# Kernel optimization log

Measured on AMD Instinct MI355X. Metric: run time of the kernel, lower is better.

The kernel has to match this reference:

```python
import jax, jax.numpy as jnp
import numpy as np
import math

B, S, D, H = 2, 2048, 2048, 16
HD = D // H  # 128


def _rope(x, cos, sin):
    # x: [b, s, h, hd]; cos/sin: [s, hd//2]
    # torch view_as_complex pairs adjacent elements: (even=real, odd=imag)
    xr = x[..., 0::2]
    xi = x[..., 1::2]
    c = cos[None, :, None, :]
    s = sin[None, :, None, :]
    out_r = xr * c - xi * s
    out_i = xr * s + xi * c
    # interleave back: [..., hd//2, 2] -> [..., hd]
    return jnp.stack([out_r, out_i], axis=-1).reshape(x.shape)


def setup_inputs() -> dict:
    key = jax.random.key(0)
    ks = jax.random.split(key, 5)
    x = jax.random.normal(ks[0], (B, S, D), dtype=jnp.float32)
    std = 1.0 / math.sqrt(D)
    wq = jax.random.normal(ks[1], (D, D), dtype=jnp.float32) * std
    wk = jax.random.normal(ks[2], (D, D), dtype=jnp.float32) * std
    wv = jax.random.normal(ks[3], (D, D), dtype=jnp.float32) * std
    wo = jax.random.normal(ks[4], (D, D), dtype=jnp.float32) * std
    # RoPE frequencies, theta = 10000
    freqs = 1.0 / (10000.0 ** (jnp.arange(0, HD, 2, dtype=jnp.float32) / HD))  # [hd//2]
    t = jnp.arange(S, dtype=jnp.float32)
    angles = jnp.outer(t, freqs)  # [s, hd//2]
    freqs_cos = jnp.cos(angles)
    freqs_sin = jnp.sin(angles)
    # causal additive mask [s, s]
    mask = jnp.triu(jnp.full((S, S), -jnp.inf, dtype=jnp.float32), k=1)
    return {"x": x, "start_pos": 0, "freqs_cos": freqs_cos, "freqs_sin": freqs_sin,
            "mask": mask, "wq": wq, "wk": wk, "wv": wv, "wo": wo}


def reference(x, start_pos, freqs_cos, freqs_sin, mask, wq, wk, wv, wo):
    b, s, d = x.shape
    # projections (torch Linear: y = x @ W.T)
    xq = (x @ wq.T).reshape(b, s, H, HD)
    xk = (x @ wk.T).reshape(b, s, H, HD)
    xv = (x @ wv.T).reshape(b, s, H, HD)
    xq = _rope(xq, freqs_cos, freqs_sin)
    xk = _rope(xk, freqs_cos, freqs_sin)
    # start_pos = 0 prefill: cache[:b, :s] == freshly computed xk/xv
    # scores: [b, h, s_q, s_k]
    scores = jnp.einsum("bqhd,bkhd->bhqk", xq, xk) / math.sqrt(HD)
    scores = scores + mask[None, None, :, :]
    probs = jax.nn.softmax(scores, axis=-1)
    out = jnp.einsum("bhqk,bkhd->bqhd", probs, xv).reshape(b, s, d)
    return out @ wo.T
```

## Files before the change

kernel.cpp:

```cpp
#include <hip/hip_runtime.h>

typedef __attribute__((ext_vector_type(8))) short short8;
typedef __attribute__((ext_vector_type(4))) float f32x4;
typedef __attribute__((ext_vector_type(16))) float f32x16;
typedef unsigned int u32;
typedef __attribute__((ext_vector_type(4))) u32 u32x4;
typedef unsigned short u16;

#define DEV __device__ __forceinline__

DEV void async16(const void* g, void* l) {
  __builtin_amdgcn_global_load_lds((const __attribute__((address_space(1))) u32*)g,
                                   (__attribute__((address_space(3))) u32*)l, 16, 0, 0);
}

DEV u16 f2bf(float f) {
  u32 u = __builtin_bit_cast(u32, f);
  u32 r = (u + 0x7FFFu + ((u >> 16) & 1u)) >> 16;
  return (u16)r;
}
DEV float bf2f(u16 h) { return __builtin_bit_cast(float, (u32)h << 16); }

DEV u32 cvtpk(float lo, float hi) {
  u32 r;
  asm("v_cvt_pk_bf16_f32 %0, %1, %2" : "=v"(r) : "v"(lo), "v"(hi));
  return r;
}

#define RAW_BARRIER() asm volatile("s_barrier" ::: "memory")
#define VMWAIT(N) asm volatile("s_waitcnt vmcnt(" #N ")" ::: "memory")

__global__ void cast_all_kernel(const float* __restrict__ x, const float* __restrict__ wq,
                                const float* __restrict__ wk, const float* __restrict__ wv,
                                const float* __restrict__ wo, u16* __restrict__ out) {
  constexpr int XN = 2097152;
  constexpr int WN = 1048576;
  constexpr int TOT = XN + 4 * WN;
  int stride = gridDim.x * blockDim.x;
  for (int i = blockIdx.x * blockDim.x + threadIdx.x; i < TOT; i += stride) {
    const float* src;
    int off;
    if (i < XN) {
      src = x; off = i;
    } else {
      int j = i - XN, wsel = j >> 20;
      const float* ws4[4] = {wq, wk, wv, wo};
      src = ws4[wsel]; off = j & (WN - 1);
    }
    float4 v = reinterpret_cast<const float4*>(src)[off];
    ushort4 o = make_ushort4(f2bf(v.x), f2bf(v.y), f2bf(v.z), f2bf(v.w));
    reinterpret_cast<ushort4*>(out)[i] = o;
  }
}

__global__ __launch_bounds__(512, 2) void gemm_qkv8(const u16* __restrict__ A,
                                                    const u16* __restrict__ Bw,
                                                    u16* __restrict__ q_ws,
                                                    u16* __restrict__ k_ws,
                                                    u16* __restrict__ vt_ws,
                                                    const float* __restrict__ cbp,
                                                    const float* __restrict__ sbp) {
  constexpr int K = 2048, NITER = 16;
  __shared__ char sm[131072];
  const int tid = threadIdx.x, lane = tid & 63, w = tid >> 6;
  const int wm = w >> 2, wn = w & 3;
  const int bid = blockIdx.x;
  const int xcd = bid & 7, jj = bid >> 3;
  const int mt = (xcd & 1) * 8 + (jj & 7);
  const int ntc = (xcd >> 1) * 6 + (jj >> 3);
  const int row0 = mt * 256, col0 = ntc * 256;

  f32x4 acc[2][2][4][2] = {};

  auto stage = [&](int slotbase, const u16* src, int rbase, int k0) {
#pragma unroll
    for (int i = 0; i < 2; ++i) {
      int slot = tid + i * 512;
      int r = slot >> 3, cs = slot & 7;
      async16(src + (size_t)(rbase + r) * K + k0 + ((cs ^ (r & 7)) << 3),
              sm + slotbase + slot * 16);
    }
  };

  short8 af[4][2], bf0[2][2], bf1[2][2];
  auto ldA = [&](int slotbase) {
#pragma unroll
    for (int mi = 0; mi < 4; ++mi) {
      int row = wm * 64 + mi * 16 + (lane & 15);
#pragma unroll
      for (int kk = 0; kk < 2; ++kk)
        af[mi][kk] = *reinterpret_cast<const short8*>(
            sm + slotbase + row * 128 + ((((kk << 2) + (lane >> 4)) ^ (row & 7)) << 4));
    }
  };
  auto ldB = [&](short8 (&bf)[2][2], int slotbase) {
#pragma unroll
    for (int ni = 0; ni < 2; ++ni) {
      int row = wn * 32 + ni * 16 + (lane & 15);
#pragma unroll
      for (int kk = 0; kk < 2; ++kk)
        bf[ni][kk] = *reinterpret_cast<const short8*>(
            sm + slotbase + row * 128 + ((((kk << 2) + (lane >> 4)) ^ (row & 7)) << 4));
    }
  };

#define MFMA16(HA, HB, BF)                                                              \
  __builtin_amdgcn_s_setprio(1);                                                        \
  _Pragma("unroll") for (int mi = 0; mi < 4; ++mi)                                      \
      _Pragma("unroll") for (int ni = 0; ni < 2; ++ni)                                  \
          _Pragma("unroll") for (int kk = 0; kk < 2; ++kk)                              \
              acc[HA][HB][mi][ni] = __builtin_amdgcn_mfma_f32_16x16x32_bf16(            \
                  af[mi][kk], BF[ni][kk], acc[HA][HB][mi][ni], 0, 0, 0);                \
  __builtin_amdgcn_s_setprio(0);

  stage(0, A, row0, 0);
  stage(32768, Bw, col0, 0);
  stage(49152, Bw, col0 + 128, 0);
  stage(16384, A, row0 + 128, 0);
  stage(65536, A, row0, 64);
  stage(65536 + 32768, Bw, col0, 64);

  for (int i = 0; i < NITER - 1; ++i) {
    const int kT1 = i * 128 + 64, kN = (i + 1) * 128;
    VMWAIT(8); RAW_BARRIER();
    ldA(0); ldB(bf0, 32768);
    stage(65536 + 49152, Bw, col0 + 128, kT1);
    MFMA16(0, 0, bf0);
    VMWAIT(8); RAW_BARRIER();
    ldB(bf1, 49152);
    stage(65536 + 16384, A, row0 + 128, kT1);
    MFMA16(0, 1, bf1);
    VMWAIT(8); RAW_BARRIER();
    ldA(16384);
    stage(0, A, row0, kN);
    stage(32768, Bw, col0, kN);
    MFMA16(1, 0, bf0);
    MFMA16(1, 1, bf1);
    VMWAIT(8); RAW_BARRIER();
    ldA(65536); ldB(bf0, 65536 + 32768);
    stage(49152, Bw, col0 + 128, kN);
    MFMA16(0, 0, bf0);
    VMWAIT(8); RAW_BARRIER();
    ldB(bf1, 65536 + 49152);
    stage(16384, A, row0 + 128, kN);
    MFMA16(0, 1, bf1);
    VMWAIT(8); RAW_BARRIER();
    ldA(65536 + 16384);
    stage(65536, A, row0, kN + 64);
    stage(65536 + 32768, Bw, col0, kN + 64);
    MFMA16(1, 0, bf0);
    MFMA16(1, 1, bf1);
  }
  {
    const int kT1 = (NITER - 1) * 128 + 64;
    VMWAIT(8); RAW_BARRIER();
    ldA(0); ldB(bf0, 32768);
    stage(65536 + 49152, Bw, col0 + 128, kT1);
    MFMA16(0, 0, bf0);
    VMWAIT(8); RAW_BARRIER();
    ldB(bf1, 49152);
    stage(65536 + 16384, A, row0 + 128, kT1);
    MFMA16(0, 1, bf1);
    VMWAIT(8); RAW_BARRIER();
    ldA(16384);
    MFMA16(1, 0, bf0);
    MFMA16(1, 1, bf1);
    VMWAIT(4); RAW_BARRIER();
    ldA(65536); ldB(bf0, 65536 + 32768);
    MFMA16(0, 0, bf0);
    VMWAIT(2); RAW_BARRIER();
    ldB(bf1, 65536 + 49152);
    MFMA16(0, 1, bf1);
    VMWAIT(0); RAW_BARRIER();
    ldA(65536 + 16384);
    MFMA16(1, 0, bf0);
    MFMA16(1, 1, bf1);
  }

  const float rs = 0.127517436f;
#pragma unroll
  for (int ha = 0; ha < 2; ++ha)
#pragma unroll
    for (int hb = 0; hb < 2; ++hb)
#pragma unroll
      for (int mi = 0; mi < 4; ++mi)
#pragma unroll
        for (int ni = 0; ni < 2; ++ni)
#pragma unroll
          for (int rr = 0; rr < 4; ++rr) {
            int gm = row0 + ha * 128 + wm * 64 + mi * 16 + ((lane >> 4) << 2) + rr;
            int gn = col0 + hb * 128 + wn * 32 + ni * 16 + (lane & 15);
            float v = acc[ha][hb][mi][ni][rr];
            int tsel = gn >> 11, nn = gn & 2047;
            int b = gm >> 11, s = gm & 2047, h = nn >> 7, hd = nn & 127;
            if (tsel < 2) {
              float pv = __shfl_xor(v, 1, 64);
              float c = cbp[(s << 6) + (hd >> 1)];
              float sn = sbp[(s << 6) + (hd >> 1)];
              float o = (hd & 1) ? (pv * sn + v * c) : (v * c - pv * sn);
              if (tsel == 0) o *= rs;
              u16* dst = tsel ? k_ws : q_ws;
              dst[(size_t)((b << 4) | h) * 262144 + (s << 7) + hd] = f2bf(o);
            } else {
              vt_ws[(size_t)((b << 4) | h) * 262144 + (hd << 11) + s] = f2bf(v);
            }
          }
#undef MFMA16
}

__global__ __launch_bounds__(256) void gemm_bt(const u16* __restrict__ A,
                                               const u16* __restrict__ Bw,
                                               float* __restrict__ C) {
  constexpr int K = 2048;
  __shared__ char sm[32768];
  const int tid = threadIdx.x;
  const int lane = tid & 63;
  const int w = tid >> 6;
  const int by = blockIdx.x & 31;
  const int bx = blockIdx.x >> 5;
  const int row0 = by * 128, col0 = bx * 128;
  const int wr = (w >> 1) * 64, wc = (w & 1) * 64;
  f32x4 acc[4][4] = {};

  for (int k0 = 0; k0 < K; k0 += 64) {
    __syncthreads();
#pragma unroll
    for (int i = 0; i < 4; ++i) {
      int slot = tid + i * 256;
      int r = slot >> 3, s = slot & 7;
      int sl = s ^ (r & 7);
      async16(A + (size_t)(row0 + r) * K + (k0 + sl * 8), sm + slot * 16);
    }
#pragma unroll
    for (int i = 0; i < 4; ++i) {
      int slot = tid + i * 256;
      int r = slot >> 3, s = slot & 7;
      int sl = s ^ (r & 7);
      async16(Bw + (size_t)(col0 + r) * K + (k0 + sl * 8), sm + 16384 + slot * 16);
    }
    __syncthreads();
#pragma unroll
    for (int kk = 0; kk < 2; ++kk) {
      short8 af[4], bfr[4];
#pragma unroll
      for (int mi = 0; mi < 4; ++mi) {
        int r = wr + mi * 16 + (lane & 15);
        int ps = (kk * 4 + (lane >> 4)) ^ (r & 7);
        af[mi] = *reinterpret_cast<const short8*>(sm + r * 128 + ps * 16);
      }
#pragma unroll
      for (int ni = 0; ni < 4; ++ni) {
        int r = wc + ni * 16 + (lane & 15);
        int ps = (kk * 4 + (lane >> 4)) ^ (r & 7);
        bfr[ni] = *reinterpret_cast<const short8*>(sm + 16384 + r * 128 + ps * 16);
      }
#pragma unroll
      for (int mi = 0; mi < 4; ++mi)
#pragma unroll
        for (int ni = 0; ni < 4; ++ni)
          acc[mi][ni] = __builtin_amdgcn_mfma_f32_16x16x32_bf16(af[mi], bfr[ni], acc[mi][ni], 0, 0, 0);
    }
  }
#pragma unroll
  for (int mi = 0; mi < 4; ++mi)
#pragma unroll
    for (int ni = 0; ni < 4; ++ni)
#pragma unroll
      for (int r = 0; r < 4; ++r) {
        int gm = row0 + wr + mi * 16 + ((lane >> 4) << 2) + r;
        int gn = col0 + wc + ni * 16 + (lane & 15);
        C[((size_t)gm << 11) + gn] = acc[mi][ni][r];
      }
}

__global__ __launch_bounds__(256, 2) void attn_kernel(const u16* __restrict__ q_ws,
                                                      const u16* __restrict__ k_ws,
                                                      const u16* __restrict__ vt_ws,
                                                      u16* __restrict__ attn_ws) {
  constexpr int S = 2048;
  constexpr float NEGBIG = -3.0e38f;
  __shared__ char sm[65536];
  const int tid = threadIdx.x, lane = tid & 63, w = tid >> 6;
  const int hi = lane >> 5, l31 = lane & 31;
  const int bid = blockIdx.x;
  const int qtr = bid >> 5;
  const int qt = (qtr < 8) ? qtr : 23 - qtr;
  const int bh = ((bid & 7) << 2) | ((bid >> 3) & 3);
  const int qr0 = qt * 128 + w * 32;
  const int ntile = 2 * qt + 2;
  const int my_nt = (qr0 >> 6) + 1;

  const u16* qp = q_ws + (size_t)bh * S * 128;
  const u16* kp = k_ws + (size_t)bh * S * 128;
  const u16* vp = vt_ws + (size_t)bh * 128 * S;

  short8 qf[8];
  {
    const u16* qr = qp + (size_t)(qr0 + l31) * 128 + hi * 8;
#pragma unroll
    for (int ks = 0; ks < 8; ++ks) qf[ks] = *reinterpret_cast<const short8*>(qr + ks * 16);
  }
  f32x16 accO[4];
#pragma unroll
  for (int dc = 0; dc < 4; ++dc)
#pragma unroll
    for (int r = 0; r < 16; ++r) accO[dc][r] = 0.f;
  float m = -1e30f, l = 0.f;

  auto stage = [&](int bufoff, int kv0) {
#pragma unroll
    for (int i = 0; i < 4; ++i) {
      int slot = tid + i * 256;
      int r = slot >> 4, s = slot & 15;
      async16(kp + (size_t)(kv0 + r) * 128 + ((s ^ (r & 15)) * 8), sm + bufoff + slot * 16);
    }
#pragma unroll
    for (int i = 0; i < 4; ++i) {
      int slot = tid + i * 256;
      int r = slot >> 3, s = slot & 7;
      async16(vp + (size_t)r * S + kv0 + ((s ^ (r & 7)) * 8), sm + bufoff + 16384 + slot * 16);
    }
  };

  stage(0, 0);
  __syncthreads();

  for (int t = 0; t < ntile; ++t) {
    const char* kb = sm + (t & 1) * 32768;
    const char* vb = kb + 16384;
    if (t + 1 < ntile) stage(((t + 1) & 1) * 32768, (t + 1) * 64);

    if (t < my_nt) {
      f32x16 sacc[2];
#pragma unroll
      for (int jc = 0; jc < 2; ++jc)
#pragma unroll
        for (int r = 0; r < 16; ++r) sacc[jc][r] = 0.f;
      __builtin_amdgcn_s_setprio(1);
#pragma unroll
      for (int jc = 0; jc < 2; ++jc) {
        const char* krp = kb + (jc * 32 + l31) * 256;
        const int sw = l31 & 15;
#pragma unroll
        for (int ks = 0; ks < 8; ++ks) {
          short8 kf = *reinterpret_cast<const short8*>(krp + (((2 * ks + hi) ^ sw) << 4));
          sacc[jc] = __builtin_amdgcn_mfma_f32_32x32x16_bf16(kf, qf[ks], sacc[jc], 0, 0, 0);
        }
      }
      __builtin_amdgcn_s_setprio(0);
      if (t == my_nt - 1) {
#pragma unroll
        for (int jc = 0; jc < 2; ++jc) {
          int thr = qr0 + l31 - t * 64 - 32 * jc - 4 * hi;
#pragma unroll
          for (int r = 0; r < 16; ++r) {
            int c0 = (r & 3) + 8 * (r >> 2);
            if (c0 > thr) sacc[jc][r] = NEGBIG;
          }
        }
      }
      float pmA = NEGBIG, pmB = NEGBIG, pmC = NEGBIG, pmD = NEGBIG;
#pragma unroll
      for (int jc = 0; jc < 2; ++jc)
#pragma unroll
        for (int r = 0; r < 16; r += 4) {
          pmA = fmaxf(pmA, sacc[jc][r]);
          pmB = fmaxf(pmB, sacc[jc][r + 1]);
          pmC = fmaxf(pmC, sacc[jc][r + 2]);
          pmD = fmaxf(pmD, sacc[jc][r + 3]);
        }
      float pmax = fmaxf(fmaxf(pmA, pmB), fmaxf(pmC, pmD));
      pmax = fmaxf(pmax, __shfl_xor(pmax, 32, 64));
      if (!__all(pmax - m <= 8.0f)) {
        float mnew = fmaxf(m, pmax);
        float scl = exp2f(m - mnew);
        m = mnew;
        l *= scl;
#pragma unroll
        for (int dc = 0; dc < 4; ++dc)
#pragma unroll
          for (int r = 0; r < 16; ++r) accO[dc][r] *= scl;
      }
      float sA = 0.f, sB = 0.f, sC = 0.f, sD = 0.f;
#pragma unroll
      for (int jc = 0; jc < 2; ++jc)
#pragma unroll
        for (int r = 0; r < 16; r += 4) {
          float p0 = exp2f(sacc[jc][r] - m);
          float p1 = exp2f(sacc[jc][r + 1] - m);
          float p2 = exp2f(sacc[jc][r + 2] - m);
          float p3 = exp2f(sacc[jc][r + 3] - m);
          sacc[jc][r] = p0; sacc[jc][r + 1] = p1; sacc[jc][r + 2] = p2; sacc[jc][r + 3] = p3;
          sA += p0; sB += p1; sC += p2; sD += p3;
        }
      float ps = (sA + sB) + (sC + sD);
      ps += __shfl_xor(ps, 32, 64);
      l += ps;
      short8 pfrag[4];
#pragma unroll
      for (int ks = 0; ks < 4; ++ks) {
        const int jc = ks >> 1, u8 = (ks & 1) * 8;
        u32 wA = cvtpk(sacc[jc][u8 + 0], sacc[jc][u8 + 1]);
        u32 wB = cvtpk(sacc[jc][u8 + 2], sacc[jc][u8 + 3]);
        u32 wC = cvtpk(sacc[jc][u8 + 4], sacc[jc][u8 + 5]);
        u32 wD = cvtpk(sacc[jc][u8 + 6], sacc[jc][u8 + 7]);
        u32 qA = __shfl_xor(wA, 32, 64);
        u32 qB = __shfl_xor(wB, 32, 64);
        u32 qC = __shfl_xor(wC, 32, 64);
        u32 qD = __shfl_xor(wD, 32, 64);
        u32x4 t4;
        t4.x = hi ? qC : wA;
        t4.y = hi ? qD : wB;
        t4.z = hi ? wC : qA;
        t4.w = hi ? wD : qB;
        pfrag[ks] = __builtin_bit_cast(short8, t4);
      }
      __builtin_amdgcn_s_setprio(1);
#pragma unroll
      for (int ks = 0; ks < 4; ++ks) {
#pragma unroll
        for (int dc = 0; dc < 4; ++dc) {
          const char* vrp = vb + (dc * 32 + l31) * 128;
          short8 vf = *reinterpret_cast<const short8*>(vrp + (((2 * ks + hi) ^ (l31 & 7)) << 4));
          accO[dc] = __builtin_amdgcn_mfma_f32_32x32x16_bf16(vf, pfrag[ks], accO[dc], 0, 0, 0);
        }
      }
      __builtin_amdgcn_s_setprio(0);
    }
    __syncthreads();
  }

  const int b = bh >> 4, h = bh & 15;
  char* tb = sm + w * 8192;
  float inv = (l > 0.f) ? 1.0f / l : 0.f;
#pragma unroll
  for (int dc = 0; dc < 4; ++dc)
#pragma unroll
    for (int r = 0; r < 16; ++r) {
      int d = dc * 32 + (r & 3) + 8 * (r >> 2) + 4 * hi;
      int byte = l31 * 256 + d * 2;
      *reinterpret_cast<u16*>(tb + (byte ^ ((l31 & 7) << 4))) = f2bf(accO[dc][r] * inv);
    }
  asm volatile("s_waitcnt lgkmcnt(0)" ::: "memory");
#pragma unroll
  for (int i = 0; i < 8; ++i) {
    int r = i * 4 + (lane >> 4);
    int s = lane & 15;
    f32x4 v = *reinterpret_cast<const f32x4*>(tb + r * 256 + ((s ^ (r & 7)) << 4));
    size_t addr = ((size_t)(b * 2048 + qr0 + r) << 11) + (h << 7) + s * 8;
    *reinterpret_cast<f32x4*>(attn_ws + addr) = v;
  }
}

extern "C" void kernel_launch(void* const* d_in, const int* in_sizes, int n_in,
                              void* d_out, int out_size, void* d_ws, size_t ws_size,
                              hipStream_t stream) {
  const float* x = (const float*)d_in[0];
  const float* cb = (const float*)d_in[2];
  const float* sb = (const float*)d_in[3];
  const float* wq = (const float*)d_in[5];
  const float* wk = (const float*)d_in[6];
  const float* wv = (const float*)d_in[7];
  const float* wo = (const float*)d_in[8];

  char* p = (char*)d_ws;
  u16* xb  = (u16*)p; p += (size_t)4096 * 2048 * 2;
  u16* wqb = (u16*)p; p += (size_t)2048 * 2048 * 2;
  u16* wkb = (u16*)p; p += (size_t)2048 * 2048 * 2;
  u16* wvb = (u16*)p; p += (size_t)2048 * 2048 * 2;
  u16* wob = (u16*)p; p += (size_t)2048 * 2048 * 2;
  u16* q_ws = (u16*)p; p += (size_t)4096 * 2048 * 2;
  u16* k_ws = (u16*)p; p += (size_t)4096 * 2048 * 2;
  u16* vt_ws = (u16*)p; p += (size_t)4096 * 2048 * 2;
  u16* attn_ws = xb;
  (void)wkb; (void)wvb;

  cast_all_kernel<<<3072, 256, 0, stream>>>(x, wq, wk, wv, wo, xb);

  gemm_qkv8<<<384, 512, 0, stream>>>(xb, wqb, q_ws, k_ws, vt_ws, cb, sb);

  attn_kernel<<<512, 256, 0, stream>>>(q_ws, k_ws, vt_ws, attn_ws);

  gemm_bt<<<512, 256, 0, stream>>>(attn_ws, wob, (float*)d_out);
}
```

Before: 293.9 us.

## Templatize 256x256 GEMM, re-pipeline LDS stages, reuse it for output projection

Turns the QKV GEMM into a template that also serves the output projection, replacing the simpler 128x128 gemm_bt with the 256x256 double-buffered kernel (128 blocks). The main loop is rescheduled into even/odd halves, with more barriers and explicit lgkmcnt waits so LDS slots are refilled right after they are read. This aims to raise MFMA utilisation in both GEMMs. The trade-off is that the output GEMM now runs only 128 large blocks, which may underfill the GPU, and the extra barriers add synchronisation cost.

```diff
diff --git a/kernel.cpp b/kernel.cpp
--- a/kernel.cpp
+++ b/kernel.cpp
@@ -27,8 +27,8 @@
   return r;
 }
 
-#define RAW_BARRIER() asm volatile("s_barrier" ::: "memory")
 #define VMWAIT(N) asm volatile("s_waitcnt vmcnt(" #N ")" ::: "memory")
+#define LGKM0() asm volatile("s_waitcnt lgkmcnt(0)" ::: "memory")
 
 __global__ void cast_all_kernel(const float* __restrict__ x, const float* __restrict__ wq,
                                 const float* __restrict__ wk, const float* __restrict__ wv,
@@ -53,22 +53,33 @@
   }
 }
 
-__global__ __launch_bounds__(512, 2) void gemm_qkv8(const u16* __restrict__ A,
-                                                    const u16* __restrict__ Bw,
-                                                    u16* __restrict__ q_ws,
-                                                    u16* __restrict__ k_ws,
-                                                    u16* __restrict__ vt_ws,
-                                                    const float* __restrict__ cbp,
-                                                    const float* __restrict__ sbp) {
+template <int MODE>
+__global__ __launch_bounds__(512, 2) void gemm256(const u16* __restrict__ A,
+                                                  const u16* __restrict__ Bw,
+                                                  void* __restrict__ C0,
+                                                  u16* __restrict__ C1,
+                                                  u16* __restrict__ C2,
+                                                  const float* __restrict__ cbp,
+                                                  const float* __restrict__ sbp) {
   constexpr int K = 2048, NITER = 16;
   __shared__ char sm[131072];
   const int tid = threadIdx.x, lane = tid & 63, w = tid >> 6;
   const int wm = w >> 2, wn = w & 3;
   const int bid = blockIdx.x;
-  const int xcd = bid & 7, jj = bid >> 3;
-  const int mt = (xcd & 1) * 8 + (jj & 7);
-  const int ntc = (xcd >> 1) * 6 + (jj >> 3);
+  int mt, ntc;
+  if constexpr (MODE == 0) {
+    const int xcd = bid & 7, jj = bid >> 3;
+    mt = (xcd & 1) * 8 + (jj & 7);
+    ntc = (xcd >> 1) * 6 + (jj >> 3);
+  } else {
+    const int xcd = bid & 7, jj = bid >> 3;
+    mt = (xcd & 1) * 8 + (jj & 7);
+    ntc = (xcd >> 1) * 2 + (jj >> 3);
+  }
   const int row0 = mt * 256, col0 = ntc * 256;
+
+  constexpr int A0e = 0, A1e = 16384, B0e = 32768, B1e = 49152;
+  constexpr int A0o = 65536, A1o = 81920, B0o = 98304, B1o = 114688;
 
   f32x4 acc[2][2][4][2] = {};
 
@@ -113,68 +124,93 @@
                   af[mi][kk], BF[ni][kk], acc[HA][HB][mi][ni], 0, 0, 0);                \
   __builtin_amdgcn_s_setprio(0);
 
-  stage(0, A, row0, 0);
-  stage(32768, Bw, col0, 0);
-  stage(49152, Bw, col0 + 128, 0);
-  stage(16384, A, row0 + 128, 0);
-  stage(65536, A, row0, 64);
-  stage(65536 + 32768, Bw, col0, 64);
+#define BAR() __builtin_amdgcn_s_barrier()
+
+  stage(A0e, A, row0, 0);
+  stage(B0e, Bw, col0, 0);
+  stage(B1e, Bw, col0 + 128, 0);
+  stage(A1e, A, row0 + 128, 0);
+  stage(A0o, A, row0, 64);
+  stage(B0o, Bw, col0, 64);
+  stage(B1o, Bw, col0 + 128, 64);
+  stage(A1o, A, row0 + 128, 64);
+  VMWAIT(8);
+  BAR();
 
   for (int i = 0; i < NITER - 1; ++i) {
-    const int kT1 = i * 128 + 64, kN = (i + 1) * 128;
-    VMWAIT(8); RAW_BARRIER();
-    ldA(0); ldB(bf0, 32768);
-    stage(65536 + 49152, Bw, col0 + 128, kT1);
+    const int kE = (i + 1) * 128, kO = kE + 64;
+    ldA(A0e); ldB(bf0, B0e);
+    BAR(); LGKM0();
     MFMA16(0, 0, bf0);
-    VMWAIT(8); RAW_BARRIER();
-    ldB(bf1, 49152);
-    stage(65536 + 16384, A, row0 + 128, kT1);
+    BAR();
+    ldB(bf1, B1e);
+    stage(A0e, A, row0, kE);
+    BAR(); LGKM0();
     MFMA16(0, 1, bf1);
-    VMWAIT(8); RAW_BARRIER();
-    ldA(16384);
-    stage(0, A, row0, kN);
-    stage(32768, Bw, col0, kN);
+    BAR();
+    ldA(A1e);
+    stage(B0e, Bw, col0, kE);
+    BAR(); LGKM0();
+    MFMA16(1, 1, bf1);
+    BAR();
+    stage(B1e, Bw, col0 + 128, kE);
+    stage(A1e, A, row0 + 128, kE);
+    BAR(); LGKM0();
     MFMA16(1, 0, bf0);
+    VMWAIT(8);
+    BAR();
+    ldA(A0o); ldB(bf0, B0o);
+    BAR(); LGKM0();
+    MFMA16(0, 0, bf0);
+    BAR();
+    ldB(bf1, B1o);
+    stage(A0o, A, row0, kO);
+    BAR(); LGKM0();
+    MFMA16(0, 1, bf1);
+    BAR();
+    ldA(A1o);
+    stage(B0o, Bw, col0, kO);
+    BAR(); LGKM0();
     MFMA16(1, 1, bf1);
-    VMWAIT(8); RAW_BARRIER();
-    ldA(65536); ldB(bf0, 65536 + 32768);
-    stage(49152, Bw, col0 + 128, kN);
+    BAR();
+    stage(B1o, Bw, col0 + 128, kO);
+    stage(A1o, A, row0 + 128, kO);
+    BAR(); LGKM0();
+    MFMA16(1, 0, bf0);
+    VMWAIT(8);
+    BAR();
+  }
+  {
+    ldA(A0e); ldB(bf0, B0e);
+    BAR(); LGKM0();
     MFMA16(0, 0, bf0);
-    VMWAIT(8); RAW_BARRIER();
-    ldB(bf1, 65536 + 49152);
-    stage(16384, A, row0 + 128, kN);
+    BAR();
+    ldB(bf1, B1e);
+    BAR(); LGKM0();
     MFMA16(0, 1, bf1);
-    VMWAIT(8); RAW_BARRIER();
-    ldA(65536 + 16384);
-    stage(65536, A, row0, kN + 64);
-    stage(65536 + 32768, Bw, col0, kN + 64);
+    BAR();
+    ldA(A1e);
+    BAR(); LGKM0();
+    MFMA16(1, 1, bf1);
+    BAR();
+    BAR(); LGKM0();
     MFMA16(1, 0, bf0);
+    VMWAIT(0);
+    BAR();
+    ldA(A0o); ldB(bf0, B0o);
+    BAR(); LGKM0();
+    MFMA16(0, 0, bf0);
+    BAR();
+    ldB(bf1, B1o);
+    BAR(); LGKM0();
+    MFMA16(0, 1, bf1);
+    BAR();
+    ldA(A1o);
+    BAR(); LGKM0();
     MFMA16(1, 1, bf1);
-  }
-  {
-    const int kT1 = (NITER - 1) * 128 + 64;
-    VMWAIT(8); RAW_BARRIER();
-    ldA(0); ldB(bf0, 32768);
-    stage(65536 + 49152, Bw, col0 + 128, kT1);
-    MFMA16(0, 0, bf0);
-    VMWAIT(8); RAW_BARRIER();
-    ldB(bf1, 49152);
-    stage(65536 + 16384, A, row0 + 128, kT1);
-    MFMA16(0, 1, bf1);
-    VMWAIT(8); RAW_BARRIER();
-    ldA(16384);
+    BAR();
+    LGKM0();
     MFMA16(1, 0, bf0);
-    MFMA16(1, 1, bf1);
-    VMWAIT(4); RAW_BARRIER();
-    ldA(65536); ldB(bf0, 65536 + 32768);
-    MFMA16(0, 0, bf0);
-    VMWAIT(2); RAW_BARRIER();
-    ldB(bf1, 65536 + 49152);
-    MFMA16(0, 1, bf1);
-    VMWAIT(0); RAW_BARRIER();
-    ldA(65536 + 16384);
-    MFMA16(1, 0, bf0);
-    MFMA16(1, 1, bf1);
   }
 
   const float rs = 0.127517436f;
@@ -191,86 +227,27 @@
             int gm = row0 + ha * 128 + wm * 64 + mi * 16 + ((lane >> 4) << 2) + rr;
             int gn = col0 + hb * 128 + wn * 32 + ni * 16 + (lane & 15);
             float v = acc[ha][hb][mi][ni][rr];
-            int tsel = gn >> 11, nn = gn & 2047;
-            int b = gm >> 11, s = gm & 2047, h = nn >> 7, hd = nn & 127;
-            if (tsel < 2) {
-              float pv = __shfl_xor(v, 1, 64);
-              float c = cbp[(s << 6) + (hd >> 1)];
-              float sn = sbp[(s << 6) + (hd >> 1)];
-              float o = (hd & 1) ? (pv * sn + v * c) : (v * c - pv * sn);
-              if (tsel == 0) o *= rs;
-              u16* dst = tsel ? k_ws : q_ws;
-              dst[(size_t)((b << 4) | h) * 262144 + (s << 7) + hd] = f2bf(o);
+            if constexpr (MODE == 0) {
+              int tsel = gn >> 11, nn = gn & 2047;
+              int b = gm >> 11, s = gm & 2047, h = nn >> 7, hd = nn & 127;
+              if (tsel < 2) {
+                float pv = __shfl_xor(v, 1, 64);
+                float c = cbp[(s << 6) + (hd >> 1)];
+                float sn = sbp[(s << 6) + (hd >> 1)];
+                float o = (hd & 1) ? (pv * sn + v * c) : (v * c - pv * sn);
+                if (tsel == 0) o *= rs;
+                u16* dst = tsel ? (u16*)C0 : C1;
+                dst = tsel ? C2 : (u16*)C0;
+                dst[(size_t)((b << 4) | h) * 262144 + (s << 7) + hd] = f2bf(o);
+              } else {
+                C1[(size_t)((b << 4) | h) * 262144 + (hd << 11) + s] = f2bf(v);
+              }
             } else {
-              vt_ws[(size_t)((b << 4) | h) * 262144 + (hd << 11) + s] = f2bf(v);
+              ((float*)C0)[((size_t)gm << 11) + gn] = v;
             }
           }
 #undef MFMA16
-}
-
-__global__ __launch_bounds__(256) void gemm_bt(const u16* __restrict__ A,
-                                               const u16* __restrict__ Bw,
-                                               float* __restrict__ C) {
-  constexpr int K = 2048;
-  __shared__ char sm[32768];
-  const int tid = threadIdx.x;
-  const int lane = tid & 63;
-  const int w = tid >> 6;
-  const int by = blockIdx.x & 31;
-  const int bx = blockIdx.x >> 5;
-  const int row0 = by * 128, col0 = bx * 128;
-  const int wr = (w >> 1) * 64, wc = (w & 1) * 64;
-  f32x4 acc[4][4] = {};
-
-  for (int k0 = 0; k0 < K; k0 += 64) {
-    __syncthreads();
-#pragma unroll
-    for (int i = 0; i < 4; ++i) {
-      int slot = tid + i * 256;
-      int r = slot >> 3, s = slot & 7;
-      int sl = s ^ (r & 7);
-      async16(A + (size_t)(row0 + r) * K + (k0 + sl * 8), sm + slot * 16);
-    }
-#pragma unroll
-    for (int i = 0; i < 4; ++i) {
-      int slot = tid + i * 256;
-      int r = slot >> 3, s = slot & 7;
-      int sl = s ^ (r & 7);
-      async16(Bw + (size_t)(col0 + r) * K + (k0 + sl * 8), sm + 16384 + slot * 16);
-    }
-    __syncthreads();
-#pragma unroll
-    for (int kk = 0; kk < 2; ++kk) {
-      short8 af[4], bfr[4];
-#pragma unroll
-      for (int mi = 0; mi < 4; ++mi) {
-        int r = wr + mi * 16 + (lane & 15);
-        int ps = (kk * 4 + (lane >> 4)) ^ (r & 7);
-        af[mi] = *reinterpret_cast<const short8*>(sm + r * 128 + ps * 16);
-      }
-#pragma unroll
-      for (int ni = 0; ni < 4; ++ni) {
-        int r = wc + ni * 16 + (lane & 15);
-        int ps = (kk * 4 + (lane >> 4)) ^ (r & 7);
-        bfr[ni] = *reinterpret_cast<const short8*>(sm + 16384 + r * 128 + ps * 16);
-      }
-#pragma unroll
-      for (int mi = 0; mi < 4; ++mi)
-#pragma unroll
-        for (int ni = 0; ni < 4; ++ni)
-          acc[mi][ni] = __builtin_amdgcn_mfma_f32_16x16x32_bf16(af[mi], bfr[ni], acc[mi][ni], 0, 0, 0);
-    }
-  }
-#pragma unroll
-  for (int mi = 0; mi < 4; ++mi)
-#pragma unroll
-    for (int ni = 0; ni < 4; ++ni)
-#pragma unroll
-      for (int r = 0; r < 4; ++r) {
-        int gm = row0 + wr + mi * 16 + ((lane >> 4) << 2) + r;
-        int gn = col0 + wc + ni * 16 + (lane & 15);
-        C[((size_t)gm << 11) + gn] = acc[mi][ni][r];
-      }
+#undef BAR
 }
 
 __global__ __launch_bounds__(256, 2) void attn_kernel(const u16* __restrict__ q_ws,
@@ -477,9 +454,9 @@
 
   cast_all_kernel<<<3072, 256, 0, stream>>>(x, wq, wk, wv, wo, xb);
 
-  gemm_qkv8<<<384, 512, 0, stream>>>(xb, wqb, q_ws, k_ws, vt_ws, cb, sb);
+  gemm256<0><<<384, 512, 0, stream>>>(xb, wqb, q_ws, vt_ws, k_ws, cb, sb);
 
   attn_kernel<<<512, 256, 0, stream>>>(q_ws, k_ws, vt_ws, attn_ws);
 
-  gemm_bt<<<512, 256, 0, stream>>>(attn_ws, wob, (float*)d_out);
-}
+  gemm256<1><<<128, 512, 0, stream>>>(attn_ws, wob, d_out, nullptr, nullptr, nullptr, nullptr);
+}
```

Result: slower. 313.3 us (+6.6%).
